# Performance work log

Hardware: AMD Instinct MI355X
Metric: run time of the kernel (lower is better)

The kernel has to match this reference:

```python
import jax, jax.numpy as jnp
import numpy as np

H, D, DS, CZ, S, B = 16, 24, 384, 128, 512, 1
EPS = 1e-5


def setup_inputs() -> dict:
    key = jax.random.key(0)
    ks = jax.random.split(key, 12)
    sc = lambda fan: 1.0 / np.sqrt(fan)
    inp = {
        's': jax.random.normal(ks[0], (B, S, DS), jnp.float32),
        'z': jax.random.normal(ks[1], (B, S, S, CZ), jnp.float32),
        'seq_mask': jnp.zeros((B, 1, 1, S), jnp.float32),
        'q_w': jax.random.normal(ks[2], (H * D, DS), jnp.float32) * sc(DS),
        'q_b': jax.random.normal(ks[3], (H * D,), jnp.float32) * 0.02,
        'k_w': jax.random.normal(ks[4], (H * D, DS), jnp.float32) * sc(DS),
        'v_w': jax.random.normal(ks[5], (H * D, DS), jnp.float32) * sc(DS),
        'g_w': jax.random.normal(ks[6], (H * D, DS), jnp.float32) * sc(DS),
        'o_w': jax.random.normal(ks[7], (DS, H * D), jnp.float32) * sc(H * D),
        'z_ln_w': jnp.ones((CZ,), jnp.float32),
        'z_ln_b': jnp.zeros((CZ,), jnp.float32),
        'z_w': jax.random.normal(ks[8], (H, CZ), jnp.float32) * sc(CZ),
    }
    return inp


def _layer_norm(x, w, b):
    mu = jnp.mean(x, axis=-1, keepdims=True)
    var = jnp.mean(jnp.square(x - mu), axis=-1, keepdims=True)
    return (x - mu) * jax.lax.rsqrt(var + EPS) * w + b


def reference(s, z, seq_mask, q_w, q_b, k_w, v_w, g_w, o_w, z_ln_w, z_ln_b, z_w):
    b, n, _ = s.shape
    # fused QKV projection (q has bias, k/v do not)
    q = (s @ q_w.T + q_b).reshape(b, n, H, D).transpose(0, 2, 1, 3)  # [B,H,S,D]
    k = (s @ k_w.T).reshape(b, n, H, D).transpose(0, 2, 1, 3)
    v = (s @ v_w.T).reshape(b, n, H, D).transpose(0, 2, 1, 3)
    # pair bias: layernorm(z) -> linear to H -> permute to [B,H,S,S]
    bias = _layer_norm(z, z_ln_w, z_ln_b) @ z_w.T          # [B,S,S,H]
    bias = bias.transpose(0, 3, 1, 2)                      # [B,H,S,S]
    bias = bias + seq_mask
    scores = jnp.einsum('bhqd,bhkd->bhqk', q, k) * (D ** -0.5) + bias
    attn = jax.nn.softmax(scores, axis=-1)
    o = jnp.einsum('bhqk,bhkd->bhqd', attn, v)             # [B,H,S,D]
    o = o.transpose(0, 2, 1, 3).reshape(b, n, H * D)
    g = jax.nn.sigmoid(s @ g_w.T)                          # gating
    return (o * g) @ o_w.T                                 # [B,S,DS]
```

## Files before the change

### kernel.cpp

```cpp
#include <hip/hip_runtime.h>

#define H 16
#define D 24
#define DS 384
#define CZ 128
#define S 512
#define EPSV 1e-5f

__global__ __launch_bounds__(256) void proj_kernel(
    const float* __restrict__ s, const float* __restrict__ q_w, const float* __restrict__ q_b,
    const float* __restrict__ k_w, const float* __restrict__ v_w, const float* __restrict__ g_w,
    float* __restrict__ Q, float* __restrict__ K, float* __restrict__ VT, float* __restrict__ G)
{
    const int b = blockIdx.x;
    const int mat = b / 48;
    const int t = b % 48;
    const int by = t / 6, bx = t % 6;
    const float* w = (mat == 0) ? q_w : (mat == 1) ? k_w : (mat == 2) ? v_w : g_w;

    __shared__ float As[32][68];
    __shared__ float Ws[32][68];

    const int tid = threadIdx.x;
    const int tx = tid & 15, ty = tid >> 4;
    const int r8 = tid >> 3;
    const int c4 = tid & 7;

    float acc[4][4] = {};
    for (int kc = 0; kc < DS; kc += 32) {
        __syncthreads();
#pragma unroll
        for (int pass = 0; pass < 2; ++pass) {
            int r = r8 + pass * 32;
            float4 sv = *(const float4*)(s + (by * 64 + r) * DS + kc + c4 * 4);
            float4 wv = *(const float4*)(w + (bx * 64 + r) * DS + kc + c4 * 4);
            As[c4 * 4 + 0][r] = sv.x; As[c4 * 4 + 1][r] = sv.y;
            As[c4 * 4 + 2][r] = sv.z; As[c4 * 4 + 3][r] = sv.w;
            Ws[c4 * 4 + 0][r] = wv.x; Ws[c4 * 4 + 1][r] = wv.y;
            Ws[c4 * 4 + 2][r] = wv.z; Ws[c4 * 4 + 3][r] = wv.w;
        }
        __syncthreads();
#pragma unroll
        for (int k = 0; k < 32; ++k) {
            float4 a4 = *(const float4*)&As[k][ty * 4];
            float4 b4 = *(const float4*)&Ws[k][tx * 4];
            acc[0][0] += a4.x * b4.x; acc[0][1] += a4.x * b4.y; acc[0][2] += a4.x * b4.z; acc[0][3] += a4.x * b4.w;
            acc[1][0] += a4.y * b4.x; acc[1][1] += a4.y * b4.y; acc[1][2] += a4.y * b4.z; acc[1][3] += a4.y * b4.w;
            acc[2][0] += a4.z * b4.x; acc[2][1] += a4.z * b4.y; acc[2][2] += a4.z * b4.z; acc[2][3] += a4.z * b4.w;
            acc[3][0] += a4.w * b4.x; acc[3][1] += a4.w * b4.y; acc[3][2] += a4.w * b4.z; acc[3][3] += a4.w * b4.w;
        }
    }

    const int r0 = by * 64 + ty * 4;
    const int c0 = bx * 64 + tx * 4;
    if (mat == 2) {
#pragma unroll
        for (int ii = 0; ii < 4; ++ii)
#pragma unroll
            for (int jj = 0; jj < 4; ++jj)
                VT[(c0 + jj) * S + (r0 + ii)] = acc[ii][jj];
    } else {
        float* dst = (mat == 0) ? Q : (mat == 1) ? K : G;
#pragma unroll
        for (int ii = 0; ii < 4; ++ii) {
            float4 v;
            v.x = acc[ii][0]; v.y = acc[ii][1]; v.z = acc[ii][2]; v.w = acc[ii][3];
            if (mat == 0) {
                v.x += q_b[c0 + 0]; v.y += q_b[c0 + 1]; v.z += q_b[c0 + 2]; v.w += q_b[c0 + 3];
            } else if (mat == 3) {
                v.x = 1.f / (1.f + __expf(-v.x)); v.y = 1.f / (1.f + __expf(-v.y));
                v.z = 1.f / (1.f + __expf(-v.z)); v.w = 1.f / (1.f + __expf(-v.w));
            }
            *(float4*)(dst + (r0 + ii) * DS + c0) = v;
        }
    }
}

__global__ __launch_bounds__(256) void score_kernel(
    const float* __restrict__ z, const float* __restrict__ seq_mask,
    const float* __restrict__ z_ln_w, const float* __restrict__ z_ln_b,
    const float* __restrict__ z_w,
    const float* __restrict__ Q, const float* __restrict__ K,
    float* __restrict__ scores)
{
    const int b = blockIdx.x;
    const int q = b >> 3;
    const int j0 = (b & 7) * 64;
    const int tid = threadIdx.x;
    const int w = tid >> 6;
    const int lane = tid & 63;

    __shared__ float a_s[H][CZ + 4];
    __shared__ float AhBh[2][H];
    __shared__ float qrow[DS];
    __shared__ float stats[4][2][68];
    __shared__ float opart[4][H][68];
    __shared__ float buf[H][68];

    {
        const int h = tid >> 4;
        const int c8 = (tid & 15) * 8;
        float A = 0.f, Bv = 0.f;
#pragma unroll
        for (int p = 0; p < 2; ++p) {
            float4 wz = *(const float4*)(z_w + h * CZ + c8 + p * 4);
            float4 lw = *(const float4*)(z_ln_w + c8 + p * 4);
            float4 lb = *(const float4*)(z_ln_b + c8 + p * 4);
            float4 a;
            a.x = lw.x * wz.x; a.y = lw.y * wz.y; a.z = lw.z * wz.z; a.w = lw.w * wz.w;
            *(float4*)&a_s[h][c8 + p * 4] = a;
            A += a.x + a.y + a.z + a.w;
            Bv += lb.x * wz.x + lb.y * wz.y + lb.z * wz.z + lb.w * wz.w;
        }
#pragma unroll
        for (int m = 1; m < 16; m <<= 1) {
            A += __shfl_xor(A, m);
            Bv += __shfl_xor(Bv, m);
        }
        if ((tid & 15) == 0) { AhBh[0][h] = A; AhBh[1][h] = Bv; }
    }
    for (int i = tid; i < DS; i += 256) qrow[i] = Q[q * DS + i];
    __syncthreads();

    {
        const int c0 = w * 32;
        const float* zr = z + ((long)q * S + j0 + lane) * CZ + c0;
        float4 zf[8];
#pragma unroll
        for (int t = 0; t < 8; ++t) zf[t] = *(const float4*)(zr + t * 4);

        float s1 = 0.f, s2 = 0.f;
#pragma unroll
        for (int t = 0; t < 8; ++t) {
            s1 += zf[t].x + zf[t].y + zf[t].z + zf[t].w;
            s2 += zf[t].x * zf[t].x + zf[t].y * zf[t].y + zf[t].z * zf[t].z + zf[t].w * zf[t].w;
        }
        stats[w][0][lane] = s1;
        stats[w][1][lane] = s2;

#pragma unroll
        for (int h = 0; h < H; ++h) {
            float acc = 0.f;
#pragma unroll
            for (int t = 0; t < 8; ++t) {
                float4 a4 = *(const float4*)&a_s[h][c0 + t * 4];
                acc += zf[t].x * a4.x + zf[t].y * a4.y + zf[t].z * a4.z + zf[t].w * a4.w;
            }
            opart[w][h][lane] = acc;
        }
    }
    __syncthreads();

    {
        const int r = tid >> 2;
        const int hq = tid & 3;
        float s1 = stats[0][0][r] + stats[1][0][r] + stats[2][0][r] + stats[3][0][r];
        float s2 = stats[0][1][r] + stats[1][1][r] + stats[2][1][r] + stats[3][1][r];
        const float mu = s1 * (1.f / 128.f);
        const float rs = rsqrtf(s2 * (1.f / 128.f) - mu * mu + EPSV);
        const float mk = seq_mask[j0 + r];
        const float scale = 0.2041241452319315f;
        const float* krow = K + (long)(j0 + r) * DS;

#pragma unroll
        for (int i = 0; i < 4; ++i) {
            const int h = hq * 4 + i;
            float dza = opart[0][h][r] + opart[1][h][r] + opart[2][h][r] + opart[3][h][r];
            const float4* k4 = (const float4*)(krow + h * D);
            const float4* q4 = (const float4*)(qrow + h * D);
            float qk = 0.f;
#pragma unroll
            for (int t = 0; t < 6; ++t) {
                float4 kv = k4[t];
                float4 qv = q4[t];
                qk += kv.x * qv.x + kv.y * qv.y + kv.z * qv.z + kv.w * qv.w;
            }
            const float bias = rs * dza - mu * rs * AhBh[0][h] + AhBh[1][h];
            buf[h][r] = qk * scale + bias + mk;
        }
    }
    __syncthreads();

    {
        const int h = tid >> 4, j4 = tid & 15;
        float4 v = *(const float4*)&buf[h][j4 * 4];
        *(float4*)(scores + ((q << 4) + h) * S + j0 + j4 * 4) = v;
    }
}

__global__ __launch_bounds__(256) void spv_kernel(
    const float* __restrict__ scores, const float* __restrict__ VT,
    const float* __restrict__ G, float* __restrict__ og)
{
    const int q = blockIdx.x;
    const int tid = threadIdx.x;
    const int wv = tid >> 6;
    const int lane = tid & 63;

    __shared__ float sc[H][S + 4];
    __shared__ float opart[4][DS];
    __shared__ float inv_l[H];

    for (int i = tid; i < H * (S / 4); i += 256) {
        int row = i >> 7, f4 = i & 127;
        float4 v = ((const float4*)(scores + ((q << 4) + row) * S))[f4];
        *(float4*)&sc[row][f4 * 4] = v;
    }
    __syncthreads();

#pragma unroll
    for (int i = 0; i < 4; ++i) {
        int h = wv * 4 + i;
        float m = -1e30f;
        for (int j = lane; j < S; j += 64) m = fmaxf(m, sc[h][j]);
#pragma unroll
        for (int mk = 1; mk < 64; mk <<= 1) m = fmaxf(m, __shfl_xor(m, mk));
        float sum = 0.f;
        for (int j = lane; j < S; j += 64) {
            float p = __expf(sc[h][j] - m);
            sc[h][j] = p;
            sum += p;
        }
#pragma unroll
        for (int mk = 1; mk < 64; mk <<= 1) sum += __shfl_xor(sum, mk);
        if (lane == 0) inv_l[h] = 1.f / sum;
    }
    __syncthreads();

#pragma unroll
    for (int ii = 0; ii < 6; ++ii) {
        int idx = ii * 64 + lane;
        int h = idx / 24;
        float acc = 0.f;
        const float4* vt4 = (const float4*)(VT + idx * S + wv * 128);
        const float4* sc4 = (const float4*)&sc[h][wv * 128];
#pragma unroll
        for (int t = 0; t < 32; ++t) {
            float4 p = sc4[t];
            float4 v = vt4[t];
            acc += p.x * v.x + p.y * v.y + p.z * v.z + p.w * v.w;
        }
        opart[wv][idx] = acc;
    }
    __syncthreads();
    for (int i = tid; i < DS; i += 256) {
        float o = opart[0][i] + opart[1][i] + opart[2][i] + opart[3][i];
        int h = i / 24;
        og[q * DS + i] = o * inv_l[h] * G[q * DS + i];
    }
}

__global__ __launch_bounds__(256) void out_kernel(
    const float* __restrict__ og, const float* __restrict__ o_w, float* __restrict__ out)
{
    const int b = blockIdx.x;
    const int by = b / 6, bx = b % 6;

    __shared__ float As[32][68];
    __shared__ float Ws[32][68];

    const int tid = threadIdx.x;
    const int tx = tid & 15, ty = tid >> 4;
    const int r8 = tid >> 3;
    const int c4 = tid & 7;

    float acc[4][4] = {};
    for (int kc = 0; kc < DS; kc += 32) {
        __syncthreads();
#pragma unroll
        for (int pass = 0; pass < 2; ++pass) {
            int r = r8 + pass * 32;
            float4 sv = *(const float4*)(og + (by * 64 + r) * DS + kc + c4 * 4);
            float4 wvv = *(const float4*)(o_w + (bx * 64 + r) * DS + kc + c4 * 4);
            As[c4 * 4 + 0][r] = sv.x; As[c4 * 4 + 1][r] = sv.y;
            As[c4 * 4 + 2][r] = sv.z; As[c4 * 4 + 3][r] = sv.w;
            Ws[c4 * 4 + 0][r] = wvv.x; Ws[c4 * 4 + 1][r] = wvv.y;
            Ws[c4 * 4 + 2][r] = wvv.z; Ws[c4 * 4 + 3][r] = wvv.w;
        }
        __syncthreads();
#pragma unroll
        for (int k = 0; k < 32; ++k) {
            float4 a4 = *(const float4*)&As[k][ty * 4];
            float4 b4 = *(const float4*)&Ws[k][tx * 4];
            acc[0][0] += a4.x * b4.x; acc[0][1] += a4.x * b4.y; acc[0][2] += a4.x * b4.z; acc[0][3] += a4.x * b4.w;
            acc[1][0] += a4.y * b4.x; acc[1][1] += a4.y * b4.y; acc[1][2] += a4.y * b4.z; acc[1][3] += a4.y * b4.w;
            acc[2][0] += a4.z * b4.x; acc[2][1] += a4.z * b4.y; acc[2][2] += a4.z * b4.z; acc[2][3] += a4.z * b4.w;
            acc[3][0] += a4.w * b4.x; acc[3][1] += a4.w * b4.y; acc[3][2] += a4.w * b4.z; acc[3][3] += a4.w * b4.w;
        }
    }

    const int r0 = by * 64 + ty * 4;
    const int c0 = bx * 64 + tx * 4;
#pragma unroll
    for (int ii = 0; ii < 4; ++ii) {
        float4 v;
        v.x = acc[ii][0]; v.y = acc[ii][1]; v.z = acc[ii][2]; v.w = acc[ii][3];
        *(float4*)(out + (r0 + ii) * DS + c0) = v;
    }
}

extern "C" void kernel_launch(void* const* d_in, const int* in_sizes, int n_in,
                              void* d_out, int out_size, void* d_ws, size_t ws_size,
                              hipStream_t stream)
{
    const float* s      = (const float*)d_in[0];
    const float* z      = (const float*)d_in[1];
    const float* mask   = (const float*)d_in[2];
    const float* q_w    = (const float*)d_in[3];
    const float* q_b    = (const float*)d_in[4];
    const float* k_w    = (const float*)d_in[5];
    const float* v_w    = (const float*)d_in[6];
    const float* g_w    = (const float*)d_in[7];
    const float* o_w    = (const float*)d_in[8];
    const float* z_ln_w = (const float*)d_in[9];
    const float* z_ln_b = (const float*)d_in[10];
    const float* z_w    = (const float*)d_in[11];

    float* Q  = (float*)d_ws;
    float* K  = Q + S * DS;
    float* VT = K + S * DS;
    float* G  = VT + S * DS;
    float* og = G + S * DS;
    float* scores = og + S * DS;

    hipLaunchKernelGGL(proj_kernel, dim3(192), dim3(256), 0, stream,
                       s, q_w, q_b, k_w, v_w, g_w, Q, K, VT, G);
    hipLaunchKernelGGL(score_kernel, dim3(4096), dim3(256), 0, stream,
                       z, mask, z_ln_w, z_ln_b, z_w, Q, K, scores);
    hipLaunchKernelGGL(spv_kernel, dim3(S), dim3(256), 0, stream,
                       scores, VT, G, og);
    hipLaunchKernelGGL(out_kernel, dim3(48), dim3(256), 0, stream,
                       og, o_w, (float*)d_out);
}
```

Before: 349.3 us.

## Restructure score kernel to one block per query row with per-wave head groups

The score kernel now launches one block per query instead of eight blocks of 64 keys each. Each wave owns four heads and loops over all 512 keys and all 128 z channels, keeping the LayerNorm statistics and the head-projection accumulators in registers. This removes the cross-wave shared-memory reductions and two barriers. In exchange, each wave re-reads the whole z row and recomputes the LayerNorm stats, which quadruples z traffic. The grid also shrinks to 512 blocks and register pressure rises.

```diff
diff --git a/kernel.cpp b/kernel.cpp
--- a/kernel.cpp
+++ b/kernel.cpp
@@ -83,19 +83,16 @@
     const float* __restrict__ Q, const float* __restrict__ K,
     float* __restrict__ scores)
 {
-    const int b = blockIdx.x;
-    const int q = b >> 3;
-    const int j0 = (b & 7) * 64;
+    const int q = blockIdx.x;
     const int tid = threadIdx.x;
     const int w = tid >> 6;
     const int lane = tid & 63;
+    const int h0 = w * 4;
 
     __shared__ float a_s[H][CZ + 4];
     __shared__ float AhBh[2][H];
     __shared__ float qrow[DS];
-    __shared__ float stats[4][2][68];
-    __shared__ float opart[4][H][68];
-    __shared__ float buf[H][68];
+    __shared__ float buf[H][S + 4];
 
     {
         const int h = tid >> 4;
@@ -122,69 +119,94 @@
     for (int i = tid; i < DS; i += 256) qrow[i] = Q[q * DS + i];
     __syncthreads();
 
-    {
-        const int c0 = w * 32;
-        const float* zr = z + ((long)q * S + j0 + lane) * CZ + c0;
-        float4 zf[8];
-#pragma unroll
-        for (int t = 0; t < 8; ++t) zf[t] = *(const float4*)(zr + t * 4);
-
-        float s1 = 0.f, s2 = 0.f;
-#pragma unroll
-        for (int t = 0; t < 8; ++t) {
-            s1 += zf[t].x + zf[t].y + zf[t].z + zf[t].w;
-            s2 += zf[t].x * zf[t].x + zf[t].y * zf[t].y + zf[t].z * zf[t].z + zf[t].w * zf[t].w;
-        }
-        stats[w][0][lane] = s1;
-        stats[w][1][lane] = s2;
-
-#pragma unroll
-        for (int h = 0; h < H; ++h) {
-            float acc = 0.f;
-#pragma unroll
-            for (int t = 0; t < 8; ++t) {
-                float4 a4 = *(const float4*)&a_s[h][c0 + t * 4];
-                acc += zf[t].x * a4.x + zf[t].y * a4.y + zf[t].z * a4.z + zf[t].w * a4.w;
+    float accz[4][8];
+    float s1[8], s2[8];
+#pragma unroll
+    for (int i = 0; i < 4; ++i)
+#pragma unroll
+        for (int bt = 0; bt < 8; ++bt) accz[i][bt] = 0.f;
+#pragma unroll
+    for (int bt = 0; bt < 8; ++bt) { s1[bt] = 0.f; s2[bt] = 0.f; }
+
+    const float* zq = z + (long)q * S * CZ;
+
+    for (int cc = 0; cc < 8; ++cc) {
+        const int c0 = cc * 16;
+        float4 areg[4][4];
+#pragma unroll
+        for (int i = 0; i < 4; ++i)
+#pragma unroll
+            for (int t = 0; t < 4; ++t)
+                areg[i][t] = *(const float4*)&a_s[h0 + i][c0 + t * 4];
+
+#pragma unroll
+        for (int bt = 0; bt < 8; ++bt) {
+            const int row = bt * 64 + lane;
+            const float4* zp = (const float4*)(zq + (long)row * CZ + c0);
+            float4 zf[4];
+#pragma unroll
+            for (int t = 0; t < 4; ++t) zf[t] = zp[t];
+#pragma unroll
+            for (int t = 0; t < 4; ++t) {
+                s1[bt] += zf[t].x + zf[t].y + zf[t].z + zf[t].w;
+                s2[bt] += zf[t].x * zf[t].x + zf[t].y * zf[t].y
+                        + zf[t].z * zf[t].z + zf[t].w * zf[t].w;
             }
-            opart[w][h][lane] = acc;
-        }
-    }
-    __syncthreads();
-
-    {
-        const int r = tid >> 2;
-        const int hq = tid & 3;
-        float s1 = stats[0][0][r] + stats[1][0][r] + stats[2][0][r] + stats[3][0][r];
-        float s2 = stats[0][1][r] + stats[1][1][r] + stats[2][1][r] + stats[3][1][r];
-        const float mu = s1 * (1.f / 128.f);
-        const float rs = rsqrtf(s2 * (1.f / 128.f) - mu * mu + EPSV);
-        const float mk = seq_mask[j0 + r];
-        const float scale = 0.2041241452319315f;
-        const float* krow = K + (long)(j0 + r) * DS;
-
+#pragma unroll
+            for (int i = 0; i < 4; ++i) {
+                float a = 0.f;
+#pragma unroll
+                for (int t = 0; t < 4; ++t)
+                    a += zf[t].x * areg[i][t].x + zf[t].y * areg[i][t].y
+                       + zf[t].z * areg[i][t].z + zf[t].w * areg[i][t].w;
+                accz[i][bt] += a;
+            }
+        }
+    }
+
+    float qk[4][8];
+#pragma unroll
+    for (int i = 0; i < 4; ++i) {
+        const int h = h0 + i;
+        float4 qreg[6];
+#pragma unroll
+        for (int t = 0; t < 6; ++t) qreg[t] = *(const float4*)&qrow[h * D + t * 4];
+#pragma unroll
+        for (int bt = 0; bt < 8; ++bt) {
+            const int row = bt * 64 + lane;
+            const float4* kp = (const float4*)(K + (long)row * DS + h * D);
+            float a = 0.f;
+#pragma unroll
+            for (int t = 0; t < 6; ++t) {
+                float4 kv = kp[t];
+                a += kv.x * qreg[t].x + kv.y * qreg[t].y + kv.z * qreg[t].z + kv.w * qreg[t].w;
+            }
+            qk[i][bt] = a;
+        }
+    }
+
+    const float scale = 0.2041241452319315f;
+#pragma unroll
+    for (int bt = 0; bt < 8; ++bt) {
+        const int row = bt * 64 + lane;
+        const float mu = s1[bt] * (1.f / 128.f);
+        const float rs = rsqrtf(s2[bt] * (1.f / 128.f) - mu * mu + EPSV);
+        const float mk = seq_mask[row];
 #pragma unroll
         for (int i = 0; i < 4; ++i) {
-            const int h = hq * 4 + i;
-            float dza = opart[0][h][r] + opart[1][h][r] + opart[2][h][r] + opart[3][h][r];
-            const float4* k4 = (const float4*)(krow + h * D);
-            const float4* q4 = (const float4*)(qrow + h * D);
-            float qk = 0.f;
-#pragma unroll
-            for (int t = 0; t < 6; ++t) {
-                float4 kv = k4[t];
-                float4 qv = q4[t];
-                qk += kv.x * qv.x + kv.y * qv.y + kv.z * qv.z + kv.w * qv.w;
-            }
-            const float bias = rs * dza - mu * rs * AhBh[0][h] + AhBh[1][h];
-            buf[h][r] = qk * scale + bias + mk;
-        }
-    }
-    __syncthreads();
-
-    {
-        const int h = tid >> 4, j4 = tid & 15;
+            const int h = h0 + i;
+            const float bias = rs * accz[i][bt] - mu * rs * AhBh[0][h] + AhBh[1][h];
+            buf[h][row] = qk[i][bt] * scale + bias + mk;
+        }
+    }
+    __syncthreads();
+
+#pragma unroll
+    for (int it = 0; it < 8; ++it) {
+        const int idx = it * 256 + tid;
+        const int h = idx >> 7, j4 = idx & 127;
         float4 v = *(const float4*)&buf[h][j4 * 4];
-        *(float4*)(scores + ((q << 4) + h) * S + j0 + j4 * 4) = v;
+        *(float4*)(scores + ((q << 4) + h) * S + j4 * 4) = v;
     }
 }
 
@@ -325,7 +347,7 @@
 
     hipLaunchKernelGGL(proj_kernel, dim3(192), dim3(256), 0, stream,
                        s, q_w, q_b, k_w, v_w, g_w, Q, K, VT, G);
-    hipLaunchKernelGGL(score_kernel, dim3(4096), dim3(256), 0, stream,
+    hipLaunchKernelGGL(score_kernel, dim3(S), dim3(256), 0, stream,
                        z, mask, z_ln_w, z_ln_b, z_w, Q, K, scores);
     hipLaunchKernelGGL(spv_kernel, dim3(S), dim3(256), 0, stream,
                        scores, VT, G, og);
```

Measured after the change: 392.5 us. 12.4% more time.

## Store V row-major and compute P·V with coalesced V row reads

Applied to the files above, without the earlier changes.

The projection kernel now writes V in its natural row-major [S, DS] layout with float4 stores, dropping the strided transposed scatter into VT. The P·V stage is restructured so each lane owns four output columns and walks 128 keys, reading contiguous V rows (coalesced across the wave) and broadcasting the probability from shared memory. Previously each lane read its own VT row of 128 floats, which produced uncoalesced strided global loads. The new loop leaves half the lanes idle for the second column group and reads smaller chunks per iteration.

```diff
diff --git a/kernel.cpp b/kernel.cpp
--- a/kernel.cpp
+++ b/kernel.cpp
@@ -10,7 +10,7 @@
 __global__ __launch_bounds__(256) void proj_kernel(
     const float* __restrict__ s, const float* __restrict__ q_w, const float* __restrict__ q_b,
     const float* __restrict__ k_w, const float* __restrict__ v_w, const float* __restrict__ g_w,
-    float* __restrict__ Q, float* __restrict__ K, float* __restrict__ VT, float* __restrict__ G)
+    float* __restrict__ Q, float* __restrict__ K, float* __restrict__ V, float* __restrict__ G)
 {
     const int b = blockIdx.x;
     const int mat = b / 48;
@@ -53,26 +53,18 @@
 
     const int r0 = by * 64 + ty * 4;
     const int c0 = bx * 64 + tx * 4;
-    if (mat == 2) {
-#pragma unroll
-        for (int ii = 0; ii < 4; ++ii)
-#pragma unroll
-            for (int jj = 0; jj < 4; ++jj)
-                VT[(c0 + jj) * S + (r0 + ii)] = acc[ii][jj];
-    } else {
-        float* dst = (mat == 0) ? Q : (mat == 1) ? K : G;
-#pragma unroll
-        for (int ii = 0; ii < 4; ++ii) {
-            float4 v;
-            v.x = acc[ii][0]; v.y = acc[ii][1]; v.z = acc[ii][2]; v.w = acc[ii][3];
-            if (mat == 0) {
-                v.x += q_b[c0 + 0]; v.y += q_b[c0 + 1]; v.z += q_b[c0 + 2]; v.w += q_b[c0 + 3];
-            } else if (mat == 3) {
-                v.x = 1.f / (1.f + __expf(-v.x)); v.y = 1.f / (1.f + __expf(-v.y));
-                v.z = 1.f / (1.f + __expf(-v.z)); v.w = 1.f / (1.f + __expf(-v.w));
-            }
-            *(float4*)(dst + (r0 + ii) * DS + c0) = v;
-        }
+    float* dst = (mat == 0) ? Q : (mat == 1) ? K : (mat == 2) ? V : G;
+#pragma unroll
+    for (int ii = 0; ii < 4; ++ii) {
+        float4 v;
+        v.x = acc[ii][0]; v.y = acc[ii][1]; v.z = acc[ii][2]; v.w = acc[ii][3];
+        if (mat == 0) {
+            v.x += q_b[c0 + 0]; v.y += q_b[c0 + 1]; v.z += q_b[c0 + 2]; v.w += q_b[c0 + 3];
+        } else if (mat == 3) {
+            v.x = 1.f / (1.f + __expf(-v.x)); v.y = 1.f / (1.f + __expf(-v.y));
+            v.z = 1.f / (1.f + __expf(-v.z)); v.w = 1.f / (1.f + __expf(-v.w));
+        }
+        *(float4*)(dst + (r0 + ii) * DS + c0) = v;
     }
 }
 
@@ -189,7 +181,7 @@
 }
 
 __global__ __launch_bounds__(256) void spv_kernel(
-    const float* __restrict__ scores, const float* __restrict__ VT,
+    const float* __restrict__ scores, const float* __restrict__ V,
     const float* __restrict__ G, float* __restrict__ og)
 {
     const int q = blockIdx.x;
@@ -227,20 +219,29 @@
     }
     __syncthreads();
 
-#pragma unroll
-    for (int ii = 0; ii < 6; ++ii) {
-        int idx = ii * 64 + lane;
-        int h = idx / 24;
-        float acc = 0.f;
-        const float4* vt4 = (const float4*)(VT + idx * S + wv * 128);
-        const float4* sc4 = (const float4*)&sc[h][wv * 128];
-#pragma unroll
-        for (int t = 0; t < 32; ++t) {
-            float4 p = sc4[t];
-            float4 v = vt4[t];
-            acc += p.x * v.x + p.y * v.y + p.z * v.z + p.w * v.w;
-        }
-        opart[wv][idx] = acc;
+    {
+        const int jb = wv * 128;
+        const int c0 = lane * 4;
+        const int h0 = c0 / 24;
+        const int c1 = 256 + lane * 4;
+        const int h1 = c1 / 24;
+        float4 a0 = {0.f, 0.f, 0.f, 0.f};
+        float4 a1 = {0.f, 0.f, 0.f, 0.f};
+#pragma unroll 4
+        for (int jj = 0; jj < 128; ++jj) {
+            const int j = jb + jj;
+            const float4* vr = (const float4*)(V + (long)j * DS);
+            const float p0 = sc[h0][j];
+            float4 v0 = vr[lane];
+            a0.x += p0 * v0.x; a0.y += p0 * v0.y; a0.z += p0 * v0.z; a0.w += p0 * v0.w;
+            if (lane < 32) {
+                const float p1 = sc[h1][j];
+                float4 v1 = vr[64 + lane];
+                a1.x += p1 * v1.x; a1.y += p1 * v1.y; a1.z += p1 * v1.z; a1.w += p1 * v1.w;
+            }
+        }
+        *(float4*)&opart[wv][c0] = a0;
+        if (lane < 32) *(float4*)&opart[wv][c1] = a1;
     }
     __syncthreads();
     for (int i = tid; i < DS; i += 256) {
@@ -318,17 +319,17 @@
 
     float* Q  = (float*)d_ws;
     float* K  = Q + S * DS;
-    float* VT = K + S * DS;
-    float* G  = VT + S * DS;
+    float* V  = K + S * DS;
+    float* G  = V + S * DS;
     float* og = G + S * DS;
     float* scores = og + S * DS;
 
     hipLaunchKernelGGL(proj_kernel, dim3(192), dim3(256), 0, stream,
-                       s, q_w, q_b, k_w, v_w, g_w, Q, K, VT, G);
+                       s, q_w, q_b, k_w, v_w, g_w, Q, K, V, G);
     hipLaunchKernelGGL(score_kernel, dim3(4096), dim3(256), 0, stream,
                        z, mask, z_ln_w, z_ln_b, z_w, Q, K, scores);
     hipLaunchKernelGGL(spv_kernel, dim3(S), dim3(256), 0, stream,
-                       scores, VT, G, og);
+                       scores, V, G, og);
     hipLaunchKernelGGL(out_kernel, dim3(48), dim3(256), 0, stream,
                        og, o_w, (float*)d_out);
 }
```

Result: faster. 338.2 us, median of 2 (-3.2%).
